# Performance work log

Measured on AMD Instinct MI355X. Metric: run time of the kernel, lower is better.

Reference implementation:

```python
import jax, jax.numpy as jnp
import numpy as np

# Dims: CrossMambaBlock(dim=256, H=32, W=32); inner Mamba(d_model=512, expand=1,
# d_state=16, bimamba_type='v2', if_devide_out=True, use_norm=True)
B, N, C = 4, 1024, 256
D_MODEL = 2 * C          # 512 (mamba d_model)
D_INNER = D_MODEL        # expand=1
D_STATE = 16
DT_RANK = 32             # ceil(512/16)
D_CONV = 4


def _ln(x, g, b, eps=1e-5):
    m = jnp.mean(x, axis=-1, keepdims=True)
    v = jnp.var(x, axis=-1, keepdims=True)
    return (x - m) * jax.lax.rsqrt(v + eps) * g + b


def _depthwise_causal_conv(x, w, b):
    # x: (B, d, L), w: (d, 1, k) -> causal conv (pad k-1 left), matches Conv1d(padding=k-1)[..., :L]
    y = jax.lax.conv_general_dilated(
        x, w, window_strides=(1,), padding=[(D_CONV - 1, 0)],
        feature_group_count=D_INNER, dimension_numbers=('NCH', 'OIH', 'NCH'))
    return y + b[None, :, None]


def _selective_scan(u, delta, A, Bm, Cm, Dv):
    # u, delta: (B, d, L); A: (d, n); Bm, Cm: (B, n, L); Dv: (d,)
    dA = jnp.exp(jnp.einsum('bdl,dn->lbdn', delta, A))
    dBu = jnp.einsum('bdl,bnl->lbdn', delta * u, Bm)
    Ct = jnp.transpose(Cm, (2, 0, 1))  # (L, B, n)

    def step(h, inp):
        dA_t, dBu_t, c_t = inp
        h = dA_t * h + dBu_t                          # (B, d, n)
        y = jnp.einsum('bdn,bn->bd', h, c_t)
        return h, y

    h0 = jnp.zeros((u.shape[0], u.shape[1], A.shape[1]), u.dtype)
    _, ys = jax.lax.scan(step, h0, (dA, dBu, Ct))
    y = jnp.transpose(ys, (1, 2, 0))                  # (B, d, L)
    return y + Dv[:, None] * u


def _mamba_dir(xz, conv_w, conv_b, xproj_w, dt_w, dt_b, A_log, Dv):
    x, z = jnp.split(xz, 2, axis=1)                   # each (B, d_inner, L)
    x = jax.nn.silu(_depthwise_causal_conv(x, conv_w, conv_b))
    x_dbl = jnp.einsum('bdl,ed->bel', x, xproj_w)     # (B, dt_rank+2n, L)
    dt = x_dbl[:, :DT_RANK]
    Bm = x_dbl[:, DT_RANK:DT_RANK + D_STATE]
    Cm = x_dbl[:, DT_RANK + D_STATE:]
    delta = jax.nn.softplus(jnp.einsum('brl,dr->bdl', dt, dt_w) + dt_b[None, :, None])
    A = -jnp.exp(A_log)
    y = _selective_scan(x, delta, A, Bm, Cm, Dv)
    return y * jax.nn.silu(z)                         # (B, d_inner, L)


def _forward(input0, input1, norm0_g, norm0_b, norm1_g, norm1_b, in_proj_w,
             convf_w, convf_b, convb_w, convb_b, xprojf_w, xprojb_w,
             dtf_w, dtf_b, dtb_w, dtb_b, A_log_f, A_log_b, D_f, D_b,
             mnorm_g, mnorm_b, outproj_w, pnorm_g, pnorm_b,
             projback_w, projback_b, cw_w, cw_b, cwln_g, cwln_b):
    i0 = jnp.nan_to_num(input0, nan=0.0, posinf=1.0, neginf=-1.0)
    i1 = jnp.nan_to_num(input1, nan=0.0, posinf=1.0, neginf=-1.0)
    skip = i0
    x0n = _ln(i0, norm0_g, norm0_b)
    x1n = _ln(i1, norm1_g, norm1_b)
    combined = jnp.concatenate([x0n, x1n], axis=-1)   # (B, N, 2C)
    weight = jax.nn.sigmoid(_ln(combined @ cw_w.T + cw_b, cwln_g, cwln_b))
    weight = jnp.clip(weight, 0.01, 0.99)
    # Mamba (bimamba v2): shared in_proj, two directional scans
    xz = jnp.einsum('bld,ed->bel', combined, in_proj_w)  # (B, 2*d_inner, L)
    out_f = _mamba_dir(xz, convf_w, convf_b, xprojf_w, dtf_w, dtf_b, A_log_f, D_f)
    out_b = _mamba_dir(jnp.flip(xz, -1), convb_w, convb_b, xprojb_w, dtb_w, dtb_b, A_log_b, D_b)
    y = (out_f + jnp.flip(out_b, -1)) * 0.5           # if_devide_out
    y = _ln(jnp.transpose(y, (0, 2, 1)), mnorm_g, mnorm_b)  # use_norm
    out = y @ outproj_w.T                              # (B, N, 2C)
    out = _ln(out, pnorm_g, pnorm_b)
    out = out @ projback_w.T + projback_b              # (B, N, C)
    out = jnp.nan_to_num(out, nan=0.0, posinf=1.0, neginf=-1.0)
    out = out * weight + x0n * (1.0 - weight)
    return out + skip


def setup_inputs() -> dict:
    key = jax.random.key(0)
    ks = iter(jax.random.split(key, 40))
    def rn(shape, s=0.02):
        return jax.random.normal(next(ks), shape, jnp.float32) * s
    inp = {}
    inp['input0'] = jax.random.normal(next(ks), (B, N, C), jnp.float32)
    inp['input1'] = jax.random.normal(next(ks), (B, N, C), jnp.float32)
    for nm in ['norm0', 'norm1']:
        inp[nm + '_g'] = jnp.ones((C,), jnp.float32)
        inp[nm + '_b'] = jnp.zeros((C,), jnp.float32)
    inp['in_proj_w'] = rn((2 * D_INNER, D_MODEL))
    for t in ['f', 'b']:
        inp['conv%s_w' % t] = rn((D_INNER, 1, D_CONV), 0.1)
        inp['conv%s_b' % t] = jnp.zeros((D_INNER,), jnp.float32)
        inp['xproj%s_w' % t] = rn((DT_RANK + 2 * D_STATE, D_INNER))
        inp['dt%s_w' % t] = rn((D_INNER, DT_RANK), 0.05)
        inp['dt%s_b' % t] = rn((D_INNER,), 0.05)
        inp['A_log_%s' % t] = jnp.log(jnp.broadcast_to(
            jnp.arange(1, D_STATE + 1, dtype=jnp.float32), (D_INNER, D_STATE)))
        inp['D_%s' % t] = jnp.ones((D_INNER,), jnp.float32)
    inp['mnorm_g'] = jnp.ones((D_INNER,), jnp.float32)
    inp['mnorm_b'] = jnp.zeros((D_INNER,), jnp.float32)
    inp['outproj_w'] = rn((D_MODEL, D_INNER))
    inp['pnorm_g'] = jnp.ones((D_MODEL,), jnp.float32)
    inp['pnorm_b'] = jnp.zeros((D_MODEL,), jnp.float32)
    inp['projback_w'] = rn((C, D_MODEL))
    inp['projback_b'] = jnp.zeros((C,), jnp.float32)
    inp['cw_w'] = rn((C, D_MODEL))
    inp['cw_b'] = jnp.zeros((C,), jnp.float32)
    inp['cwln_g'] = jnp.ones((C,), jnp.float32)
    inp['cwln_b'] = jnp.zeros((C,), jnp.float32)
    return inp


def reference(input0, input1, norm0_g, norm0_b, norm1_g, norm1_b, in_proj_w,
              convf_w, convf_b, convb_w, convb_b, xprojf_w, xprojb_w,
              dtf_w, dtf_b, dtb_w, dtb_b, A_log_f, A_log_b, D_f, D_b,
              mnorm_g, mnorm_b, outproj_w, pnorm_g, pnorm_b,
              projback_w, projback_b, cw_w, cw_b, cwln_g, cwln_b):
    return _forward(input0, input1, norm0_g, norm0_b, norm1_g, norm1_b, in_proj_w,
                    convf_w, convf_b, convb_w, convb_b, xprojf_w, xprojb_w,
                    dtf_w, dtf_b, dtb_w, dtb_b, A_log_f, A_log_b, D_f, D_b,
                    mnorm_g, mnorm_b, outproj_w, pnorm_g, pnorm_b,
                    projback_w, projback_b, cw_w, cw_b, cwln_g, cwln_b)
```

## Files before the change

kernel.cpp:

```cpp
#include <hip/hip_runtime.h>

#define BDIM 4
#define SEQ 1024
#define CH 256
#define DMODEL 512
#define DINNER 512
#define DSTATE 16
#define DTRANK 32
#define NROWS (BDIM * SEQ)
#define NCHUNK 32
#define CHUNK (SEQ / NCHUNK)

typedef unsigned short ushort_t;

__device__ __forceinline__ float nan2num(float x) {
    if (isnan(x)) return 0.f;
    if (isinf(x)) return x > 0.f ? 1.f : -1.f;
    return x;
}

__device__ __forceinline__ float silu_f(float x) { return x / (1.f + __expf(-x)); }
__device__ __forceinline__ float sigmoid_f(float x) { return 1.f / (1.f + __expf(-x)); }
__device__ __forceinline__ float softplus_f(float x) {
    return x > 20.f ? x : log1pf(__expf(x));
}

__device__ __forceinline__ ushort_t f2bf(float x) {
    union { float f; unsigned u; } v; v.f = x;
    unsigned r = v.u + 0x7fff + ((v.u >> 16) & 1);
    return (ushort_t)(r >> 16);
}
__device__ __forceinline__ float bf2f(ushort_t x) {
    union { unsigned u; float f; } v; v.u = ((unsigned)x) << 16;
    return v.f;
}

using bf16x8 = __attribute__((ext_vector_type(8))) __bf16;
using f32x4  = __attribute__((ext_vector_type(4))) float;

__device__ __forceinline__ void wave_reduce2(float& s, float& q) {
#pragma unroll
    for (int m = 32; m > 0; m >>= 1) {
        s += __shfl_xor(s, m);
        q += __shfl_xor(q, m);
    }
}

#define SZ_INPROJ (1024 * 512)
#define SZ_CW     (256 * 512)
#define SZ_XP     (64 * 512)
#define SZ_DT     (512 * 32)
#define SZ_OUTP   (512 * 512)
#define SZ_PROJB  (256 * 512)
#define SZ_WTOT   (SZ_INPROJ + SZ_CW + 2 * SZ_XP + 2 * SZ_DT + SZ_OUTP + SZ_PROJB)

__global__ __launch_bounds__(256) void convert_weights_kernel(
        const float* __restrict__ w0, const float* __restrict__ w1,
        const float* __restrict__ w2, const float* __restrict__ w3,
        const float* __restrict__ w4, const float* __restrict__ w5,
        const float* __restrict__ w6, const float* __restrict__ w7,
        ushort_t* __restrict__ out) {
    int i = blockIdx.x * 256 + threadIdx.x;
    if (i >= SZ_WTOT) return;
    int j = i;
    const float* src;
    if (j < SZ_INPROJ) { src = w0; }
    else { j -= SZ_INPROJ;
        if (j < SZ_CW) { src = w1; }
        else { j -= SZ_CW;
            if (j < SZ_XP) { src = w2; }
            else { j -= SZ_XP;
                if (j < SZ_XP) { src = w3; }
                else { j -= SZ_XP;
                    if (j < SZ_DT) { src = w4; }
                    else { j -= SZ_DT;
                        if (j < SZ_DT) { src = w5; }
                        else { j -= SZ_DT;
                            if (j < SZ_OUTP) { src = w6; }
                            else { j -= SZ_OUTP; src = w7; }
                        }
                    }
                }
            }
        }
    }
    out[i] = f2bf(src[j]);
}

__global__ __launch_bounds__(256) void ln01_kernel(
        const float* __restrict__ i0, const float* __restrict__ i1,
        const float* __restrict__ g0, const float* __restrict__ b0,
        const float* __restrict__ g1, const float* __restrict__ b1,
        float* __restrict__ x0n, ushort_t* __restrict__ combined) {
    int w = threadIdx.x >> 6, lane = threadIdx.x & 63;
    int row = blockIdx.x * 4 + w;

    float4 v = ((const float4*)(i0 + row * CH))[lane];
    v.x = nan2num(v.x); v.y = nan2num(v.y); v.z = nan2num(v.z); v.w = nan2num(v.w);
    float s = v.x + v.y + v.z + v.w;
    float q = v.x * v.x + v.y * v.y + v.z * v.z + v.w * v.w;
    wave_reduce2(s, q);
    float m = s / (float)CH;
    float r = rsqrtf(q / (float)CH - m * m + 1e-5f);
    float4 g = ((const float4*)g0)[lane];
    float4 bb = ((const float4*)b0)[lane];
    float4 o;
    o.x = (v.x - m) * r * g.x + bb.x;
    o.y = (v.y - m) * r * g.y + bb.y;
    o.z = (v.z - m) * r * g.z + bb.z;
    o.w = (v.w - m) * r * g.w + bb.w;
    ((float4*)(x0n + row * CH))[lane] = o;
    *(ushort4*)(combined + row * DMODEL + lane * 4) =
        make_ushort4(f2bf(o.x), f2bf(o.y), f2bf(o.z), f2bf(o.w));

    v = ((const float4*)(i1 + row * CH))[lane];
    v.x = nan2num(v.x); v.y = nan2num(v.y); v.z = nan2num(v.z); v.w = nan2num(v.w);
    s = v.x + v.y + v.z + v.w;
    q = v.x * v.x + v.y * v.y + v.z * v.z + v.w * v.w;
    wave_reduce2(s, q);
    m = s / (float)CH;
    r = rsqrtf(q / (float)CH - m * m + 1e-5f);
    g = ((const float4*)g1)[lane];
    bb = ((const float4*)b1)[lane];
    o.x = (v.x - m) * r * g.x + bb.x;
    o.y = (v.y - m) * r * g.y + bb.y;
    o.z = (v.z - m) * r * g.z + bb.z;
    o.w = (v.w - m) * r * g.w + bb.w;
    *(ushort4*)(combined + row * DMODEL + CH + lane * 4) =
        make_ushort4(f2bf(o.x), f2bf(o.y), f2bf(o.z), f2bf(o.w));
}

template<int ACT>
__global__ __launch_bounds__(256) void gemm64_kernel(
        const ushort_t* __restrict__ A0, const ushort_t* __restrict__ A1, int lda,
        const ushort_t* __restrict__ W0, const ushort_t* __restrict__ W1, int ldw,
        ushort_t* __restrict__ C0, ushort_t* __restrict__ C1, int ldc,
        int K, const float* __restrict__ bias0, const float* __restrict__ bias1) {
    const ushort_t* A = blockIdx.z ? A1 : A0;
    const ushort_t* W = blockIdx.z ? W1 : W0;
    ushort_t* C = blockIdx.z ? C1 : C0;
    const float* bias = blockIdx.z ? bias1 : bias0;

    __shared__ __align__(16) ushort_t As[64][40];
    __shared__ __align__(16) ushort_t Ws[64][40];
    const int t = threadIdx.x;
    const int m0 = blockIdx.y * 64;
    const int n0 = blockIdx.x * 64;
    const int w = t >> 6;
    const int lane = t & 63;
    const int lane16 = lane & 15;
    const int quad = lane >> 4;
    const int wr = (w >> 1) * 32;
    const int wc = (w & 1) * 32;
    const int srow = t >> 2;
    const int sc8 = (t & 3) * 8;

    f32x4 acc[2][2] = {};

    for (int k0 = 0; k0 < K; k0 += 32) {
        float4 av = *(const float4*)(A + (m0 + srow) * lda + k0 + sc8);
        float4 wv = *(const float4*)(W + (n0 + srow) * ldw + k0 + sc8);
        *(float4*)&As[srow][sc8] = av;
        *(float4*)&Ws[srow][sc8] = wv;
        __syncthreads();

        bf16x8 af[2], bfr[2];
#pragma unroll
        for (int i = 0; i < 2; ++i) {
            af[i]  = *(bf16x8*)&As[wr + i * 16 + lane16][quad * 8];
            bfr[i] = *(bf16x8*)&Ws[wc + i * 16 + lane16][quad * 8];
        }
#pragma unroll
        for (int i = 0; i < 2; ++i)
#pragma unroll
            for (int j = 0; j < 2; ++j)
                acc[i][j] = __builtin_amdgcn_mfma_f32_16x16x32_bf16(af[i], bfr[j], acc[i][j], 0, 0, 0);
        __syncthreads();
    }

#pragma unroll
    for (int j = 0; j < 2; ++j) {
        int col = n0 + wc + j * 16 + lane16;
        float bv = bias ? bias[col] : 0.f;
#pragma unroll
        for (int i = 0; i < 2; ++i) {
#pragma unroll
            for (int r = 0; r < 4; ++r) {
                int row = m0 + wr + i * 16 + quad * 4 + r;
                float c = acc[i][j][r] + bv;
                if (ACT == 1) c = softplus_f(c);
                C[row * ldc + col] = f2bf(c);
            }
        }
    }
}

template<int ACT>
__global__ __launch_bounds__(256) void gemm128_kernel(
        const ushort_t* __restrict__ A0, const ushort_t* __restrict__ A1, int lda,
        const ushort_t* __restrict__ W0, const ushort_t* __restrict__ W1, int ldw,
        ushort_t* __restrict__ C0, ushort_t* __restrict__ C1, int ldc,
        int K, const float* __restrict__ bias0, const float* __restrict__ bias1) {
    const ushort_t* A = blockIdx.z ? A1 : A0;
    const ushort_t* W = blockIdx.z ? W1 : W0;
    ushort_t* C = blockIdx.z ? C1 : C0;
    const float* bias = blockIdx.z ? bias1 : bias0;

    __shared__ __align__(16) ushort_t As[128][40];
    __shared__ __align__(16) ushort_t Ws[64][40];
    const int t = threadIdx.x;
    const int m0 = blockIdx.y * 128;
    const int n0 = blockIdx.x * 64;
    const int w = t >> 6;
    const int lane = t & 63;
    const int lane16 = lane & 15;
    const int quad = lane >> 4;
    const int wr = (w >> 1) * 64;
    const int wc = (w & 1) * 32;
    const int arow = t >> 1;
    const int ac = (t & 1) * 16;
    const int srow = t >> 2;
    const int sc8 = (t & 3) * 8;

    f32x4 acc[4][2] = {};

    for (int k0 = 0; k0 < K; k0 += 32) {
        float4 a0 = *(const float4*)(A + (m0 + arow) * lda + k0 + ac);
        float4 a1 = *(const float4*)(A + (m0 + arow) * lda + k0 + ac + 8);
        float4 wv = *(const float4*)(W + (n0 + srow) * ldw + k0 + sc8);
        *(float4*)&As[arow][ac] = a0;
        *(float4*)&As[arow][ac + 8] = a1;
        *(float4*)&Ws[srow][sc8] = wv;
        __syncthreads();

        bf16x8 af[4], bfr[2];
#pragma unroll
        for (int i = 0; i < 4; ++i)
            af[i] = *(bf16x8*)&As[wr + i * 16 + lane16][quad * 8];
#pragma unroll
        for (int j = 0; j < 2; ++j)
            bfr[j] = *(bf16x8*)&Ws[wc + j * 16 + lane16][quad * 8];
#pragma unroll
        for (int i = 0; i < 4; ++i)
#pragma unroll
            for (int j = 0; j < 2; ++j)
                acc[i][j] = __builtin_amdgcn_mfma_f32_16x16x32_bf16(af[i], bfr[j], acc[i][j], 0, 0, 0);
        __syncthreads();
    }

#pragma unroll
    for (int j = 0; j < 2; ++j) {
        int col = n0 + wc + j * 16 + lane16;
        float bv = bias ? bias[col] : 0.f;
#pragma unroll
        for (int i = 0; i < 4; ++i) {
#pragma unroll
            for (int r = 0; r < 4; ++r) {
                int row = m0 + wr + i * 16 + quad * 4 + r;
                float c = acc[i][j][r] + bv;
                if (ACT == 1) c = softplus_f(c);
                C[row * ldc + col] = f2bf(c);
            }
        }
    }
}

__global__ __launch_bounds__(256) void gemm_projback_final_kernel(
        const ushort_t* __restrict__ A, int lda,
        const ushort_t* __restrict__ W, int ldw,
        int K, const float* __restrict__ bias,
        const ushort_t* __restrict__ wgt, const float* __restrict__ x0n,
        const float* __restrict__ i0, float* __restrict__ out) {
    __shared__ __align__(16) ushort_t As[64][40];
    __shared__ __align__(16) ushort_t Ws[64][40];
    const int t = threadIdx.x;
    const int m0 = blockIdx.y * 64;
    const int n0 = blockIdx.x * 64;
    const int w = t >> 6;
    const int lane = t & 63;
    const int lane16 = lane & 15;
    const int quad = lane >> 4;
    const int wr = (w >> 1) * 32;
    const int wc = (w & 1) * 32;
    const int srow = t >> 2;
    const int sc8 = (t & 3) * 8;

    f32x4 acc[2][2] = {};

    for (int k0 = 0; k0 < K; k0 += 32) {
        float4 av = *(const float4*)(A + (m0 + srow) * lda + k0 + sc8);
        float4 wv = *(const float4*)(W + (n0 + srow) * ldw + k0 + sc8);
        *(float4*)&As[srow][sc8] = av;
        *(float4*)&Ws[srow][sc8] = wv;
        __syncthreads();

        bf16x8 af[2], bfr[2];
#pragma unroll
        for (int i = 0; i < 2; ++i) {
            af[i]  = *(bf16x8*)&As[wr + i * 16 + lane16][quad * 8];
            bfr[i] = *(bf16x8*)&Ws[wc + i * 16 + lane16][quad * 8];
        }
#pragma unroll
        for (int i = 0; i < 2; ++i)
#pragma unroll
            for (int j = 0; j < 2; ++j)
                acc[i][j] = __builtin_amdgcn_mfma_f32_16x16x32_bf16(af[i], bfr[j], acc[i][j], 0, 0, 0);
        __syncthreads();
    }

#pragma unroll
    for (int j = 0; j < 2; ++j) {
        int col = n0 + wc + j * 16 + lane16;
        float bv = bias[col];
#pragma unroll
        for (int i = 0; i < 2; ++i) {
#pragma unroll
            for (int r = 0; r < 4; ++r) {
                int row = m0 + wr + i * 16 + quad * 4 + r;
                float o = nan2num(acc[i][j][r] + bv);
                float wv = bf2f(wgt[row * CH + col]);
                float xv = x0n[row * CH + col];
                float sk = nan2num(i0[row * CH + col]);
                out[row * CH + col] = o * wv + xv * (1.f - wv) + sk;
            }
        }
    }
}

__global__ __launch_bounds__(256) void weight_ln_kernel(
        ushort_t* __restrict__ wbuf, const float* __restrict__ g, const float* __restrict__ b) {
    int w = threadIdx.x >> 6, lane = threadIdx.x & 63;
    int row = blockIdx.x * 4 + w;
    ushort4 raw = *(const ushort4*)(wbuf + row * CH + lane * 4);
    float4 v = make_float4(bf2f(raw.x), bf2f(raw.y), bf2f(raw.z), bf2f(raw.w));
    float s = v.x + v.y + v.z + v.w;
    float q = v.x * v.x + v.y * v.y + v.z * v.z + v.w * v.w;
    wave_reduce2(s, q);
    float m = s / (float)CH;
    float r = rsqrtf(q / (float)CH - m * m + 1e-5f);
    float4 g4 = ((const float4*)g)[lane];
    float4 b4 = ((const float4*)b)[lane];
    float ox = fminf(fmaxf(sigmoid_f((v.x - m) * r * g4.x + b4.x), 0.01f), 0.99f);
    float oy = fminf(fmaxf(sigmoid_f((v.y - m) * r * g4.y + b4.y), 0.01f), 0.99f);
    float oz = fminf(fmaxf(sigmoid_f((v.z - m) * r * g4.z + b4.z), 0.01f), 0.99f);
    float ow = fminf(fmaxf(sigmoid_f((v.w - m) * r * g4.w + b4.w), 0.01f), 0.99f);
    *(ushort4*)(wbuf + row * CH + lane * 4) = make_ushort4(f2bf(ox), f2bf(oy), f2bf(oz), f2bf(ow));
}

__global__ __launch_bounds__(256) void conv_both_kernel(
        const ushort_t* __restrict__ xz,
        const float* __restrict__ wf, const float* __restrict__ wbf,
        const float* __restrict__ wb, const float* __restrict__ wbb,
        ushort_t* __restrict__ outf, ushort_t* __restrict__ outb) {
    const int t = threadIdx.x;
    const int lane = t & 127;
    const int row = blockIdx.x * 2 + (t >> 7);
    const int l = row & (SEQ - 1);
    const int b = row >> 10;
    const int d0 = lane * 4;

    float x[7][4];
#pragma unroll
    for (int j = 0; j < 7; ++j) {
        int ll = l - 3 + j;
        if (ll >= 0 && ll < SEQ) {
            ushort4 raw = *(const ushort4*)(xz + (b * SEQ + ll) * (2 * DINNER) + d0);
            x[j][0] = bf2f(raw.x); x[j][1] = bf2f(raw.y);
            x[j][2] = bf2f(raw.z); x[j][3] = bf2f(raw.w);
        } else {
#pragma unroll
            for (int k = 0; k < 4; ++k) x[j][k] = 0.f;
        }
    }

    float wfv[16], wbv[16];
#pragma unroll
    for (int qq = 0; qq < 4; ++qq) {
        float4 a = *(const float4*)(wf + d0 * 4 + qq * 4);
        wfv[qq * 4] = a.x; wfv[qq * 4 + 1] = a.y; wfv[qq * 4 + 2] = a.z; wfv[qq * 4 + 3] = a.w;
        float4 c = *(const float4*)(wb + d0 * 4 + qq * 4);
        wbv[qq * 4] = c.x; wbv[qq * 4 + 1] = c.y; wbv[qq * 4 + 2] = c.z; wbv[qq * 4 + 3] = c.w;
    }
    float4 bfv = *(const float4*)(wbf + d0);
    float4 bbv = *(const float4*)(wbb + d0);
    float biasf[4] = {bfv.x, bfv.y, bfv.z, bfv.w};
    float biasb[4] = {bbv.x, bbv.y, bbv.z, bbv.w};

    ushort_t of[4], ob[4];
#pragma unroll
    for (int qq = 0; qq < 4; ++qq) {
        float accf = biasf[qq], accb = biasb[qq];
#pragma unroll
        for (int k = 0; k < 4; ++k) {
            accf += x[k][qq] * wfv[qq * 4 + k];
            accb += x[6 - k][qq] * wbv[qq * 4 + k];
        }
        of[qq] = f2bf(silu_f(accf));
        ob[qq] = f2bf(silu_f(accb));
    }
    *(ushort4*)(outf + row * DINNER + d0) = make_ushort4(of[0], of[1], of[2], of[3]);
    *(ushort4*)(outb + (b * SEQ + (SEQ - 1 - l)) * DINNER + d0) =
        make_ushort4(ob[0], ob[1], ob[2], ob[3]);
}

__global__ __launch_bounds__(256) void scan_pass1_kernel(
        const ushort_t* __restrict__ df, const ushort_t* __restrict__ db,
        const ushort_t* __restrict__ uf, const ushort_t* __restrict__ ub,
        const ushort_t* __restrict__ xf, const ushort_t* __restrict__ xb,
        const float* __restrict__ Alf, const float* __restrict__ Alb,
        float* __restrict__ cAf, float* __restrict__ cAb,
        float* __restrict__ cHf, float* __restrict__ cHb) {
    const int dir = blockIdx.z >> 2;
    const int b = blockIdx.z & 3;
    const ushort_t* delta = dir ? db : df;
    const ushort_t* u     = dir ? ub : uf;
    const ushort_t* xdbl  = dir ? xb : xf;
    const float* A_log    = dir ? Alb : Alf;
    float* chunkA = dir ? cAb : cAf;
    float* chunkH = dir ? cHb : cHf;

    const int c = blockIdx.y;
    const int d = blockIdx.x * 256 + threadIdx.x;
    const int base = b * SEQ + c * CHUNK;

    __shared__ float sB[CHUNK][16];
    {
        int t = threadIdx.x;
        if (t < CHUNK * 2) {
            int row = t >> 1, f8 = (t & 1) * 8;
            float4 raw = *(const float4*)(xdbl + (base + row) * 64 + DTRANK + f8);
            const ushort_t* us = (const ushort_t*)&raw;
#pragma unroll
            for (int k = 0; k < 8; ++k) sB[row][f8 + k] = bf2f(us[k]);
        }
    }
    __syncthreads();

    float a[DSTATE];
#pragma unroll
    for (int n = 0; n < DSTATE; n += 4) {
        float4 al = *(const float4*)(A_log + d * DSTATE + n);
        a[n] = -__expf(al.x); a[n + 1] = -__expf(al.y);
        a[n + 2] = -__expf(al.z); a[n + 3] = -__expf(al.w);
    }
    float h[DSTATE];
#pragma unroll
    for (int n = 0; n < DSTATE; ++n) h[n] = 0.f;

    float sumdl = 0.f;
    for (int s = 0; s < CHUNK; ++s) {
        int row = base + s;
        float dl = bf2f(delta[row * DINNER + d]);
        float ul = bf2f(u[row * DINNER + d]);
        float dlul = dl * ul;
        sumdl += dl;
#pragma unroll
        for (int g = 0; g < 4; ++g) {
            float4 B4 = *(const float4*)&sB[s][g * 4];
            float dA0 = __expf(dl * a[g * 4 + 0]);
            float dA1 = __expf(dl * a[g * 4 + 1]);
            float dA2 = __expf(dl * a[g * 4 + 2]);
            float dA3 = __expf(dl * a[g * 4 + 3]);
            h[g * 4 + 0] = dA0 * h[g * 4 + 0] + dlul * B4.x;
            h[g * 4 + 1] = dA1 * h[g * 4 + 1] + dlul * B4.y;
            h[g * 4 + 2] = dA2 * h[g * 4 + 2] + dlul * B4.z;
            h[g * 4 + 3] = dA3 * h[g * 4 + 3] + dlul * B4.w;
        }
    }

    int idx = ((b * NCHUNK + c) * DINNER + d) * DSTATE;
#pragma unroll
    for (int n = 0; n < DSTATE; n += 4) {
        float4 P4 = make_float4(__expf(a[n] * sumdl), __expf(a[n + 1] * sumdl),
                                __expf(a[n + 2] * sumdl), __expf(a[n + 3] * sumdl));
        *(float4*)(chunkA + idx + n) = P4;
        *(float4*)(chunkH + idx + n) = make_float4(h[n], h[n + 1], h[n + 2], h[n + 3]);
    }
}

__global__ __launch_bounds__(256) void scan_pass2_kernel(
        const float* __restrict__ cAf, const float* __restrict__ cAb,
        float* __restrict__ cHf, float* __restrict__ cHb) {
    int tid = blockIdx.x * 256 + threadIdx.x;
    int dir = tid >> 15;
    int rr = tid & 32767;
    int b = rr >> 13;
    int rem = rr & 8191;
    const float* chunkA = dir ? cAb : cAf;
    float* chunkH = dir ? cHb : cHf;
    float h = 0.f;
    for (int c = 0; c < NCHUNK; ++c) {
        int idx = (b * NCHUNK + c) * (DINNER * DSTATE) + rem;
        float Ac = chunkA[idx];
        float Hc = chunkH[idx];
        chunkH[idx] = h;
        h = Ac * h + Hc;
    }
}

__global__ __launch_bounds__(256) void scan_pass3_kernel(
        const ushort_t* __restrict__ df, const ushort_t* __restrict__ db,
        const ushort_t* __restrict__ uf, const ushort_t* __restrict__ ub,
        const ushort_t* __restrict__ xf, const ushort_t* __restrict__ xb,
        const float* __restrict__ Alf, const float* __restrict__ Alb,
        const float* __restrict__ Dvf, const float* __restrict__ Dvb,
        const float* __restrict__ hfb, const float* __restrict__ hbb,
        ushort_t* __restrict__ yfo, ushort_t* __restrict__ ybo) {
    const int dir = blockIdx.z >> 2;
    const int b = blockIdx.z & 3;
    const ushort_t* delta = dir ? db : df;
    const ushort_t* u     = dir ? ub : uf;
    const ushort_t* xdbl  = dir ? xb : xf;
    const float* A_log    = dir ? Alb : Alf;
    const float* Dv       = dir ? Dvb : Dvf;
    const float* hin      = dir ? hbb : hfb;
    ushort_t* yout        = dir ? ybo : yfo;

    const int c = blockIdx.y;
    const int d = blockIdx.x * 256 + threadIdx.x;
    const int base = b * SEQ + c * CHUNK;

    __shared__ float sBC[CHUNK][32];
    {
        int t = threadIdx.x;
        if (t < CHUNK * 4) {
            int row = t >> 2, f8 = (t & 3) * 8;
            float4 raw = *(const float4*)(xdbl + (base + row) * 64 + DTRANK + f8);
            const ushort_t* us = (const ushort_t*)&raw;
#pragma unroll
            for (int k = 0; k < 8; ++k) sBC[row][f8 + k] = bf2f(us[k]);
        }
    }
    __syncthreads();

    float a[DSTATE];
#pragma unroll
    for (int n = 0; n < DSTATE; n += 4) {
        float4 al = *(const float4*)(A_log + d * DSTATE + n);
        a[n] = -__expf(al.x); a[n + 1] = -__expf(al.y);
        a[n + 2] = -__expf(al.z); a[n + 3] = -__expf(al.w);
    }
    float h[DSTATE];
    {
        int idx = ((b * NCHUNK + c) * DINNER + d) * DSTATE;
#pragma unroll
        for (int n = 0; n < DSTATE; n += 4) {
            float4 h4 = *(const float4*)(hin + idx + n);
            h[n] = h4.x; h[n + 1] = h4.y; h[n + 2] = h4.z; h[n + 3] = h4.w;
        }
    }
    const float Dd = Dv[d];

    for (int s = 0; s < CHUNK; ++s) {
        int row = base + s;
        float dl = bf2f(delta[row * DINNER + d]);
        float ul = bf2f(u[row * DINNER + d]);
        float dlul = dl * ul;
        float y = 0.f;
#pragma unroll
        for (int g = 0; g < 4; ++g) {
            float4 B4 = *(const float4*)&sBC[s][g * 4];
            float4 C4 = *(const float4*)&sBC[s][16 + g * 4];
            float dA0 = __expf(dl * a[g * 4 + 0]);
            float dA1 = __expf(dl * a[g * 4 + 1]);
            float dA2 = __expf(dl * a[g * 4 + 2]);
            float dA3 = __expf(dl * a[g * 4 + 3]);
            h[g * 4 + 0] = dA0 * h[g * 4 + 0] + dlul * B4.x;
            h[g * 4 + 1] = dA1 * h[g * 4 + 1] + dlul * B4.y;
            h[g * 4 + 2] = dA2 * h[g * 4 + 2] + dlul * B4.z;
            h[g * 4 + 3] = dA3 * h[g * 4 + 3] + dlul * B4.w;
            y += h[g * 4 + 0] * C4.x + h[g * 4 + 1] * C4.y
               + h[g * 4 + 2] * C4.z + h[g * 4 + 3] * C4.w;
        }
        int lpos = c * CHUNK + s;
        int orow = b * SEQ + (dir ? (SEQ - 1 - lpos) : lpos);
        yout[orow * DINNER + d] = f2bf(y + Dd * ul);
    }
}

__global__ __launch_bounds__(256) void combine_mnorm_kernel(
        const ushort_t* __restrict__ yf, const ushort_t* __restrict__ yb,
        const ushort_t* __restrict__ xz,
        const float* __restrict__ g, const float* __restrict__ b,
        ushort_t* __restrict__ yn) {
    int w = threadIdx.x >> 6, lane = threadIdx.x & 63;
    int row = blockIdx.x * 4 + w;
    float4 rf = *(const float4*)(yf + row * DINNER + lane * 8);
    float4 rb = *(const float4*)(yb + row * DINNER + lane * 8);
    float4 rz = *(const float4*)(xz + row * (2 * DINNER) + DINNER + lane * 8);
    const ushort_t* uf = (const ushort_t*)&rf;
    const ushort_t* ub = (const ushort_t*)&rb;
    const ushort_t* uz = (const ushort_t*)&rz;
    float v[8];
    float s = 0.f, q = 0.f;
#pragma unroll
    for (int k = 0; k < 8; ++k) {
        float val = 0.5f * (bf2f(uf[k]) + bf2f(ub[k])) * silu_f(bf2f(uz[k]));
        v[k] = val; s += val; q += val * val;
    }
    wave_reduce2(s, q);
    float m = s / (float)DINNER;
    float r = rsqrtf(q / (float)DINNER - m * m + 1e-5f);
    ushort_t o[8];
#pragma unroll
    for (int k = 0; k < 8; ++k)
        o[k] = f2bf((v[k] - m) * r * g[lane * 8 + k] + b[lane * 8 + k]);
    *(ushort4*)(yn + row * DINNER + lane * 8) = make_ushort4(o[0], o[1], o[2], o[3]);
    *(ushort4*)(yn + row * DINNER + lane * 8 + 4) = make_ushort4(o[4], o[5], o[6], o[7]);
}

__global__ __launch_bounds__(256) void ln512_kernel(
        const ushort_t* __restrict__ in,
        const float* __restrict__ g, const float* __restrict__ b,
        ushort_t* __restrict__ out) {
    int w = threadIdx.x >> 6, lane = threadIdx.x & 63;
    int row = blockIdx.x * 4 + w;
    float4 raw = *(const float4*)(in + row * DMODEL + lane * 8);
    const ushort_t* us = (const ushort_t*)&raw;
    float v[8];
    float s = 0.f, q = 0.f;
#pragma unroll
    for (int k = 0; k < 8; ++k) {
        v[k] = bf2f(us[k]); s += v[k]; q += v[k] * v[k];
    }
    wave_reduce2(s, q);
    float m = s / (float)DMODEL;
    float r = rsqrtf(q / (float)DMODEL - m * m + 1e-5f);
    ushort_t o[8];
#pragma unroll
    for (int k = 0; k < 8; ++k)
        o[k] = f2bf((v[k] - m) * r * g[lane * 8 + k] + b[lane * 8 + k]);
    *(ushort4*)(out + row * DMODEL + lane * 8) = make_ushort4(o[0], o[1], o[2], o[3]);
    *(ushort4*)(out + row * DMODEL + lane * 8 + 4) = make_ushort4(o[4], o[5], o[6], o[7]);
}

extern "C" void kernel_launch(void* const* d_in, const int* in_sizes, int n_in,
                              void* d_out, int out_size, void* d_ws, size_t ws_size,
                              hipStream_t stream) {
    (void)in_sizes; (void)n_in; (void)out_size; (void)ws_size;
    const float* input0    = (const float*)d_in[0];
    const float* input1    = (const float*)d_in[1];
    const float* norm0_g   = (const float*)d_in[2];
    const float* norm0_b   = (const float*)d_in[3];
    const float* norm1_g   = (const float*)d_in[4];
    const float* norm1_b   = (const float*)d_in[5];
    const float* in_proj_w = (const float*)d_in[6];
    const float* convf_w   = (const float*)d_in[7];
    const float* convf_b   = (const float*)d_in[8];
    const float* xprojf_w  = (const float*)d_in[9];
    const float* dtf_w     = (const float*)d_in[10];
    const float* dtf_b     = (const float*)d_in[11];
    const float* A_log_f   = (const float*)d_in[12];
    const float* D_f       = (const float*)d_in[13];
    const float* convb_w   = (const float*)d_in[14];
    const float* convb_b   = (const float*)d_in[15];
    const float* xprojb_w  = (const float*)d_in[16];
    const float* dtb_w     = (const float*)d_in[17];
    const float* dtb_b     = (const float*)d_in[18];
    const float* A_log_b   = (const float*)d_in[19];
    const float* D_b       = (const float*)d_in[20];
    const float* mnorm_g   = (const float*)d_in[21];
    const float* mnorm_b   = (const float*)d_in[22];
    const float* outproj_w = (const float*)d_in[23];
    const float* pnorm_g   = (const float*)d_in[24];
    const float* pnorm_b   = (const float*)d_in[25];
    const float* projback_w= (const float*)d_in[26];
    const float* projback_b= (const float*)d_in[27];
    const float* cw_w      = (const float*)d_in[28];
    const float* cw_b      = (const float*)d_in[29];
    const float* cwln_g    = (const float*)d_in[30];
    const float* cwln_b    = (const float*)d_in[31];

    float* wsf = (float*)d_ws;
    float* x0n      = wsf;
    float* chunkA_f = x0n + 1048576;
    float* chunkA_b = chunkA_f + 1048576;
    float* chunkH_f = chunkA_b + 1048576;
    float* chunkH_b = chunkH_f + 1048576;
    ushort_t* wsu = (ushort_t*)(chunkH_b + 1048576);
    ushort_t* combined = wsu;
    ushort_t* xz       = combined + 2097152;
    ushort_t* weight   = xz + 4194304;
    ushort_t* xdbl_f   = weight + 1048576;
    ushort_t* xdbl_b   = xdbl_f + 262144;
    ushort_t* xconv_f  = xdbl_b + 262144;
    ushort_t* xconv_b  = xconv_f + 2097152;
    ushort_t* delta_f  = xconv_b + 2097152;
    ushort_t* delta_b  = delta_f + 2097152;
    ushort_t* y_f      = delta_b + 2097152;
    ushort_t* y_b      = y_f + 2097152;
    ushort_t* yn       = y_b + 2097152;
    ushort_t* o1       = yn + 2097152;
    ushort_t* on1      = o1 + 2097152;
    ushort_t* wb       = on1 + 2097152;
    ushort_t* w_inproj = wb;
    ushort_t* w_cw     = w_inproj + SZ_INPROJ;
    ushort_t* w_xpf    = w_cw + SZ_CW;
    ushort_t* w_xpb    = w_xpf + SZ_XP;
    ushort_t* w_dtf    = w_xpb + SZ_XP;
    ushort_t* w_dtb    = w_dtf + SZ_DT;
    ushort_t* w_outp   = w_dtb + SZ_DT;
    ushort_t* w_projb  = w_outp + SZ_OUTP;

    convert_weights_kernel<<<(SZ_WTOT + 255) / 256, 256, 0, stream>>>(
        in_proj_w, cw_w, xprojf_w, xprojb_w, dtf_w, dtb_w, outproj_w, projback_w, wb);

    ln01_kernel<<<NROWS / 4, 256, 0, stream>>>(input0, input1, norm0_g, norm0_b,
                                               norm1_g, norm1_b, x0n, combined);

    gemm128_kernel<0><<<dim3(16, 32, 1), 256, 0, stream>>>(
        combined, combined, DMODEL, w_inproj, w_inproj, DMODEL,
        xz, xz, 2 * DINNER, DMODEL, nullptr, nullptr);

    gemm64_kernel<0><<<dim3(4, 64, 1), 256, 0, stream>>>(
        combined, combined, DMODEL, w_cw, w_cw, DMODEL,
        weight, weight, CH, DMODEL, cw_b, cw_b);

    weight_ln_kernel<<<NROWS / 4, 256, 0, stream>>>(weight, cwln_g, cwln_b);

    conv_both_kernel<<<NROWS / 2, 256, 0, stream>>>(
        xz, convf_w, convf_b, convb_w, convb_b, xconv_f, xconv_b);

    gemm64_kernel<0><<<dim3(1, 64, 2), 256, 0, stream>>>(
        xconv_f, xconv_b, DINNER, w_xpf, w_xpb, DINNER,
        xdbl_f, xdbl_b, 64, DINNER, nullptr, nullptr);

    gemm128_kernel<1><<<dim3(8, 32, 2), 256, 0, stream>>>(
        xdbl_f, xdbl_b, 64, w_dtf, w_dtb, DTRANK,
        delta_f, delta_b, DINNER, DTRANK, dtf_b, dtb_b);

    dim3 sgrid(DINNER / 256, NCHUNK, 2 * BDIM);
    scan_pass1_kernel<<<sgrid, 256, 0, stream>>>(
        delta_f, delta_b, xconv_f, xconv_b, xdbl_f, xdbl_b, A_log_f, A_log_b,
        chunkA_f, chunkA_b, chunkH_f, chunkH_b);
    scan_pass2_kernel<<<256, 256, 0, stream>>>(chunkA_f, chunkA_b, chunkH_f, chunkH_b);
    scan_pass3_kernel<<<sgrid, 256, 0, stream>>>(
        delta_f, delta_b, xconv_f, xconv_b, xdbl_f, xdbl_b, A_log_f, A_log_b,
        D_f, D_b, chunkH_f, chunkH_b, y_f, y_b);

    combine_mnorm_kernel<<<NROWS / 4, 256, 0, stream>>>(y_f, y_b, xz, mnorm_g, mnorm_b, yn);

    gemm128_kernel<0><<<dim3(8, 32, 1), 256, 0, stream>>>(
        yn, yn, DINNER, w_outp, w_outp, DINNER,
        o1, o1, DMODEL, DINNER, nullptr, nullptr);

    ln512_kernel<<<NROWS / 4, 256, 0, stream>>>(o1, pnorm_g, pnorm_b, on1);

    gemm_projback_final_kernel<<<dim3(4, 64, 1), 256, 0, stream>>>(
        on1, DMODEL, w_projb, DMODEL, DMODEL, projback_b,
        weight, x0n, input0, (float*)d_out);
}
```

Baseline: 270.6 us.

## Fuse delta projection into scan passes and merge small pre-processing launches

The dt-projection GEMM and softplus are now computed inside both scan passes from the xdbl rows staged in shared memory, so the bf16 delta buffers are never written or read. The weight conversion and input LayerNorm share one launch, the in_proj and cw GEMMs share one launch through the z dimension with an early exit for the narrower one, and the weight LayerNorm is folded into the conv launch. This removes several launches and a large intermediate round trip, at the cost of recomputing the 32-wide dot product in both pass1 and pass3 and holding 32 extra registers per thread.

```diff
diff --git a/kernel.cpp b/kernel.cpp
--- a/kernel.cpp
+++ b/kernel.cpp
@@ -53,45 +53,48 @@
 #define SZ_OUTP   (512 * 512)
 #define SZ_PROJB  (256 * 512)
 #define SZ_WTOT   (SZ_INPROJ + SZ_CW + 2 * SZ_XP + 2 * SZ_DT + SZ_OUTP + SZ_PROJB)
-
-__global__ __launch_bounds__(256) void convert_weights_kernel(
+#define LN01_BLOCKS (NROWS / 4)
+#define CVT_BLOCKS  ((SZ_WTOT + 255) / 256)
+
+__global__ __launch_bounds__(256) void fused_pre_kernel(
+        const float* __restrict__ i0, const float* __restrict__ i1,
+        const float* __restrict__ g0, const float* __restrict__ b0,
+        const float* __restrict__ g1, const float* __restrict__ b1,
+        float* __restrict__ x0n, ushort_t* __restrict__ combined,
         const float* __restrict__ w0, const float* __restrict__ w1,
         const float* __restrict__ w2, const float* __restrict__ w3,
         const float* __restrict__ w4, const float* __restrict__ w5,
         const float* __restrict__ w6, const float* __restrict__ w7,
-        ushort_t* __restrict__ out) {
-    int i = blockIdx.x * 256 + threadIdx.x;
-    if (i >= SZ_WTOT) return;
-    int j = i;
-    const float* src;
-    if (j < SZ_INPROJ) { src = w0; }
-    else { j -= SZ_INPROJ;
-        if (j < SZ_CW) { src = w1; }
-        else { j -= SZ_CW;
-            if (j < SZ_XP) { src = w2; }
-            else { j -= SZ_XP;
-                if (j < SZ_XP) { src = w3; }
+        ushort_t* __restrict__ wout) {
+    if (blockIdx.x >= LN01_BLOCKS) {
+        int i = (blockIdx.x - LN01_BLOCKS) * 256 + threadIdx.x;
+        if (i >= SZ_WTOT) return;
+        int j = i;
+        const float* src;
+        if (j < SZ_INPROJ) { src = w0; }
+        else { j -= SZ_INPROJ;
+            if (j < SZ_CW) { src = w1; }
+            else { j -= SZ_CW;
+                if (j < SZ_XP) { src = w2; }
                 else { j -= SZ_XP;
-                    if (j < SZ_DT) { src = w4; }
-                    else { j -= SZ_DT;
-                        if (j < SZ_DT) { src = w5; }
+                    if (j < SZ_XP) { src = w3; }
+                    else { j -= SZ_XP;
+                        if (j < SZ_DT) { src = w4; }
                         else { j -= SZ_DT;
-                            if (j < SZ_OUTP) { src = w6; }
-                            else { j -= SZ_OUTP; src = w7; }
+                            if (j < SZ_DT) { src = w5; }
+                            else { j -= SZ_DT;
+                                if (j < SZ_OUTP) { src = w6; }
+                                else { j -= SZ_OUTP; src = w7; }
+                            }
                         }
                     }
                 }
             }
         }
-    }
-    out[i] = f2bf(src[j]);
-}
-
-__global__ __launch_bounds__(256) void ln01_kernel(
-        const float* __restrict__ i0, const float* __restrict__ i1,
-        const float* __restrict__ g0, const float* __restrict__ b0,
-        const float* __restrict__ g1, const float* __restrict__ b1,
-        float* __restrict__ x0n, ushort_t* __restrict__ combined) {
+        wout[i] = f2bf(src[j]);
+        return;
+    }
+
     int w = threadIdx.x >> 6, lane = threadIdx.x & 63;
     int row = blockIdx.x * 4 + w;
 
@@ -131,79 +134,17 @@
 }
 
 template<int ACT>
-__global__ __launch_bounds__(256) void gemm64_kernel(
+__global__ __launch_bounds__(256) void gemm128_kernel(
         const ushort_t* __restrict__ A0, const ushort_t* __restrict__ A1, int lda,
         const ushort_t* __restrict__ W0, const ushort_t* __restrict__ W1, int ldw,
-        ushort_t* __restrict__ C0, ushort_t* __restrict__ C1, int ldc,
-        int K, const float* __restrict__ bias0, const float* __restrict__ bias1) {
+        ushort_t* __restrict__ C0, ushort_t* __restrict__ C1, int ldc0, int ldc1,
+        int K, const float* __restrict__ bias0, const float* __restrict__ bias1,
+        int nx1) {
+    if (blockIdx.z && (int)blockIdx.x >= nx1) return;
     const ushort_t* A = blockIdx.z ? A1 : A0;
     const ushort_t* W = blockIdx.z ? W1 : W0;
     ushort_t* C = blockIdx.z ? C1 : C0;
-    const float* bias = blockIdx.z ? bias1 : bias0;
-
-    __shared__ __align__(16) ushort_t As[64][40];
-    __shared__ __align__(16) ushort_t Ws[64][40];
-    const int t = threadIdx.x;
-    const int m0 = blockIdx.y * 64;
-    const int n0 = blockIdx.x * 64;
-    const int w = t >> 6;
-    const int lane = t & 63;
-    const int lane16 = lane & 15;
-    const int quad = lane >> 4;
-    const int wr = (w >> 1) * 32;
-    const int wc = (w & 1) * 32;
-    const int srow = t >> 2;
-    const int sc8 = (t & 3) * 8;
-
-    f32x4 acc[2][2] = {};
-
-    for (int k0 = 0; k0 < K; k0 += 32) {
-        float4 av = *(const float4*)(A + (m0 + srow) * lda + k0 + sc8);
-        float4 wv = *(const float4*)(W + (n0 + srow) * ldw + k0 + sc8);
-        *(float4*)&As[srow][sc8] = av;
-        *(float4*)&Ws[srow][sc8] = wv;
-        __syncthreads();
-
-        bf16x8 af[2], bfr[2];
-#pragma unroll
-        for (int i = 0; i < 2; ++i) {
-            af[i]  = *(bf16x8*)&As[wr + i * 16 + lane16][quad * 8];
-            bfr[i] = *(bf16x8*)&Ws[wc + i * 16 + lane16][quad * 8];
-        }
-#pragma unroll
-        for (int i = 0; i < 2; ++i)
-#pragma unroll
-            for (int j = 0; j < 2; ++j)
-                acc[i][j] = __builtin_amdgcn_mfma_f32_16x16x32_bf16(af[i], bfr[j], acc[i][j], 0, 0, 0);
-        __syncthreads();
-    }
-
-#pragma unroll
-    for (int j = 0; j < 2; ++j) {
-        int col = n0 + wc + j * 16 + lane16;
-        float bv = bias ? bias[col] : 0.f;
-#pragma unroll
-        for (int i = 0; i < 2; ++i) {
-#pragma unroll
-            for (int r = 0; r < 4; ++r) {
-                int row = m0 + wr + i * 16 + quad * 4 + r;
-                float c = acc[i][j][r] + bv;
-                if (ACT == 1) c = softplus_f(c);
-                C[row * ldc + col] = f2bf(c);
-            }
-        }
-    }
-}
-
-template<int ACT>
-__global__ __launch_bounds__(256) void gemm128_kernel(
-        const ushort_t* __restrict__ A0, const ushort_t* __restrict__ A1, int lda,
-        const ushort_t* __restrict__ W0, const ushort_t* __restrict__ W1, int ldw,
-        ushort_t* __restrict__ C0, ushort_t* __restrict__ C1, int ldc,
-        int K, const float* __restrict__ bias0, const float* __restrict__ bias1) {
-    const ushort_t* A = blockIdx.z ? A1 : A0;
-    const ushort_t* W = blockIdx.z ? W1 : W0;
-    ushort_t* C = blockIdx.z ? C1 : C0;
+    const int ldc = blockIdx.z ? ldc1 : ldc0;
     const float* bias = blockIdx.z ? bias1 : bias0;
 
     __shared__ __align__(16) ushort_t As[128][40];
@@ -254,6 +195,71 @@
         float bv = bias ? bias[col] : 0.f;
 #pragma unroll
         for (int i = 0; i < 4; ++i) {
+#pragma unroll
+            for (int r = 0; r < 4; ++r) {
+                int row = m0 + wr + i * 16 + quad * 4 + r;
+                float c = acc[i][j][r] + bv;
+                if (ACT == 1) c = softplus_f(c);
+                C[row * ldc + col] = f2bf(c);
+            }
+        }
+    }
+}
+
+template<int ACT>
+__global__ __launch_bounds__(256) void gemm64_kernel(
+        const ushort_t* __restrict__ A0, const ushort_t* __restrict__ A1, int lda,
+        const ushort_t* __restrict__ W0, const ushort_t* __restrict__ W1, int ldw,
+        ushort_t* __restrict__ C0, ushort_t* __restrict__ C1, int ldc,
+        int K, const float* __restrict__ bias0, const float* __restrict__ bias1) {
+    const ushort_t* A = blockIdx.z ? A1 : A0;
+    const ushort_t* W = blockIdx.z ? W1 : W0;
+    ushort_t* C = blockIdx.z ? C1 : C0;
+    const float* bias = blockIdx.z ? bias1 : bias0;
+
+    __shared__ __align__(16) ushort_t As[64][40];
+    __shared__ __align__(16) ushort_t Ws[64][40];
+    const int t = threadIdx.x;
+    const int m0 = blockIdx.y * 64;
+    const int n0 = blockIdx.x * 64;
+    const int w = t >> 6;
+    const int lane = t & 63;
+    const int lane16 = lane & 15;
+    const int quad = lane >> 4;
+    const int wr = (w >> 1) * 32;
+    const int wc = (w & 1) * 32;
+    const int srow = t >> 2;
+    const int sc8 = (t & 3) * 8;
+
+    f32x4 acc[2][2] = {};
+
+    for (int k0 = 0; k0 < K; k0 += 32) {
+        float4 av = *(const float4*)(A + (m0 + srow) * lda + k0 + sc8);
+        float4 wv = *(const float4*)(W + (n0 + srow) * ldw + k0 + sc8);
+        *(float4*)&As[srow][sc8] = av;
+        *(float4*)&Ws[srow][sc8] = wv;
+        __syncthreads();
+
+        bf16x8 af[2], bfr[2];
+#pragma unroll
+        for (int i = 0; i < 2; ++i) {
+            af[i]  = *(bf16x8*)&As[wr + i * 16 + lane16][quad * 8];
+            bfr[i] = *(bf16x8*)&Ws[wc + i * 16 + lane16][quad * 8];
+        }
+#pragma unroll
+        for (int i = 0; i < 2; ++i)
+#pragma unroll
+            for (int j = 0; j < 2; ++j)
+                acc[i][j] = __builtin_amdgcn_mfma_f32_16x16x32_bf16(af[i], bfr[j], acc[i][j], 0, 0, 0);
+        __syncthreads();
+    }
+
+#pragma unroll
+    for (int j = 0; j < 2; ++j) {
+        int col = n0 + wc + j * 16 + lane16;
+        float bv = bias ? bias[col] : 0.f;
+#pragma unroll
+        for (int i = 0; i < 2; ++i) {
 #pragma unroll
             for (int r = 0; r < 4; ++r) {
                 int row = m0 + wr + i * 16 + quad * 4 + r;
@@ -327,32 +333,33 @@
     }
 }
 
-__global__ __launch_bounds__(256) void weight_ln_kernel(
-        ushort_t* __restrict__ wbuf, const float* __restrict__ g, const float* __restrict__ b) {
-    int w = threadIdx.x >> 6, lane = threadIdx.x & 63;
-    int row = blockIdx.x * 4 + w;
-    ushort4 raw = *(const ushort4*)(wbuf + row * CH + lane * 4);
-    float4 v = make_float4(bf2f(raw.x), bf2f(raw.y), bf2f(raw.z), bf2f(raw.w));
-    float s = v.x + v.y + v.z + v.w;
-    float q = v.x * v.x + v.y * v.y + v.z * v.z + v.w * v.w;
-    wave_reduce2(s, q);
-    float m = s / (float)CH;
-    float r = rsqrtf(q / (float)CH - m * m + 1e-5f);
-    float4 g4 = ((const float4*)g)[lane];
-    float4 b4 = ((const float4*)b)[lane];
-    float ox = fminf(fmaxf(sigmoid_f((v.x - m) * r * g4.x + b4.x), 0.01f), 0.99f);
-    float oy = fminf(fmaxf(sigmoid_f((v.y - m) * r * g4.y + b4.y), 0.01f), 0.99f);
-    float oz = fminf(fmaxf(sigmoid_f((v.z - m) * r * g4.z + b4.z), 0.01f), 0.99f);
-    float ow = fminf(fmaxf(sigmoid_f((v.w - m) * r * g4.w + b4.w), 0.01f), 0.99f);
-    *(ushort4*)(wbuf + row * CH + lane * 4) = make_ushort4(f2bf(ox), f2bf(oy), f2bf(oz), f2bf(ow));
-}
-
-__global__ __launch_bounds__(256) void conv_both_kernel(
+__global__ __launch_bounds__(256) void conv_wln_kernel(
         const ushort_t* __restrict__ xz,
         const float* __restrict__ wf, const float* __restrict__ wbf,
         const float* __restrict__ wb, const float* __restrict__ wbb,
-        ushort_t* __restrict__ outf, ushort_t* __restrict__ outb) {
+        ushort_t* __restrict__ outf, ushort_t* __restrict__ outb,
+        ushort_t* __restrict__ wbuf, const float* __restrict__ cg,
+        const float* __restrict__ cb) {
     const int t = threadIdx.x;
+    if (blockIdx.x >= NROWS / 2) {
+        int w = t >> 6, lane = t & 63;
+        int row = (blockIdx.x - NROWS / 2) * 4 + w;
+        ushort4 raw = *(const ushort4*)(wbuf + row * CH + lane * 4);
+        float4 v = make_float4(bf2f(raw.x), bf2f(raw.y), bf2f(raw.z), bf2f(raw.w));
+        float s = v.x + v.y + v.z + v.w;
+        float q = v.x * v.x + v.y * v.y + v.z * v.z + v.w * v.w;
+        wave_reduce2(s, q);
+        float m = s / (float)CH;
+        float r = rsqrtf(q / (float)CH - m * m + 1e-5f);
+        float4 g4 = ((const float4*)cg)[lane];
+        float4 b4 = ((const float4*)cb)[lane];
+        float ox = fminf(fmaxf(sigmoid_f((v.x - m) * r * g4.x + b4.x), 0.01f), 0.99f);
+        float oy = fminf(fmaxf(sigmoid_f((v.y - m) * r * g4.y + b4.y), 0.01f), 0.99f);
+        float oz = fminf(fmaxf(sigmoid_f((v.z - m) * r * g4.z + b4.z), 0.01f), 0.99f);
+        float ow = fminf(fmaxf(sigmoid_f((v.w - m) * r * g4.w + b4.w), 0.01f), 0.99f);
+        *(ushort4*)(wbuf + row * CH + lane * 4) = make_ushort4(f2bf(ox), f2bf(oy), f2bf(oz), f2bf(ow));
+        return;
+    }
     const int lane = t & 127;
     const int row = blockIdx.x * 2 + (t >> 7);
     const int l = row & (SEQ - 1);
@@ -404,18 +411,20 @@
 }
 
 __global__ __launch_bounds__(256) void scan_pass1_kernel(
-        const ushort_t* __restrict__ df, const ushort_t* __restrict__ db,
         const ushort_t* __restrict__ uf, const ushort_t* __restrict__ ub,
         const ushort_t* __restrict__ xf, const ushort_t* __restrict__ xb,
+        const ushort_t* __restrict__ dtwf, const ushort_t* __restrict__ dtwb,
+        const float* __restrict__ dtbf, const float* __restrict__ dtbb,
         const float* __restrict__ Alf, const float* __restrict__ Alb,
         float* __restrict__ cAf, float* __restrict__ cAb,
         float* __restrict__ cHf, float* __restrict__ cHb) {
     const int dir = blockIdx.z >> 2;
     const int b = blockIdx.z & 3;
-    const ushort_t* delta = dir ? db : df;
-    const ushort_t* u     = dir ? ub : uf;
-    const ushort_t* xdbl  = dir ? xb : xf;
-    const float* A_log    = dir ? Alb : Alf;
+    const ushort_t* u    = dir ? ub : uf;
+    const ushort_t* xdbl = dir ? xb : xf;
+    const ushort_t* dtw  = dir ? dtwb : dtwf;
+    const float* dtbias  = dir ? dtbb : dtbf;
+    const float* A_log   = dir ? Alb : Alf;
     float* chunkA = dir ? cAb : cAf;
     float* chunkH = dir ? cHb : cHf;
 
@@ -423,18 +432,26 @@
     const int d = blockIdx.x * 256 + threadIdx.x;
     const int base = b * SEQ + c * CHUNK;
 
-    __shared__ float sB[CHUNK][16];
+    __shared__ float sX[CHUNK][64];
     {
         int t = threadIdx.x;
-        if (t < CHUNK * 2) {
-            int row = t >> 1, f8 = (t & 1) * 8;
-            float4 raw = *(const float4*)(xdbl + (base + row) * 64 + DTRANK + f8);
-            const ushort_t* us = (const ushort_t*)&raw;
-#pragma unroll
-            for (int k = 0; k < 8; ++k) sB[row][f8 + k] = bf2f(us[k]);
-        }
+        int row = t >> 3, oct = (t & 7) * 8;
+        float4 raw = *(const float4*)(xdbl + (base + row) * 64 + oct);
+        const ushort_t* us = (const ushort_t*)&raw;
+#pragma unroll
+        for (int k = 0; k < 8; ++k) sX[row][oct + k] = bf2f(us[k]);
     }
     __syncthreads();
+
+    float dtv[32];
+#pragma unroll
+    for (int r8 = 0; r8 < 4; ++r8) {
+        float4 raw = *(const float4*)(dtw + d * DTRANK + r8 * 8);
+        const ushort_t* us = (const ushort_t*)&raw;
+#pragma unroll
+        for (int k = 0; k < 8; ++k) dtv[r8 * 8 + k] = bf2f(us[k]);
+    }
+    const float dtb0 = dtbias[d];
 
     float a[DSTATE];
 #pragma unroll
@@ -449,14 +466,20 @@
 
     float sumdl = 0.f;
     for (int s = 0; s < CHUNK; ++s) {
-        int row = base + s;
-        float dl = bf2f(delta[row * DINNER + d]);
-        float ul = bf2f(u[row * DINNER + d]);
+        float acc = dtb0;
+#pragma unroll
+        for (int g = 0; g < 8; ++g) {
+            float4 xr = *(const float4*)&sX[s][g * 4];
+            acc += xr.x * dtv[g * 4] + xr.y * dtv[g * 4 + 1]
+                 + xr.z * dtv[g * 4 + 2] + xr.w * dtv[g * 4 + 3];
+        }
+        float dl = softplus_f(acc);
+        float ul = bf2f(u[(base + s) * DINNER + d]);
         float dlul = dl * ul;
         sumdl += dl;
 #pragma unroll
         for (int g = 0; g < 4; ++g) {
-            float4 B4 = *(const float4*)&sB[s][g * 4];
+            float4 B4 = *(const float4*)&sX[s][32 + g * 4];
             float dA0 = __expf(dl * a[g * 4 + 0]);
             float dA1 = __expf(dl * a[g * 4 + 1]);
             float dA2 = __expf(dl * a[g * 4 + 2]);
@@ -499,39 +522,49 @@
 }
 
 __global__ __launch_bounds__(256) void scan_pass3_kernel(
-        const ushort_t* __restrict__ df, const ushort_t* __restrict__ db,
         const ushort_t* __restrict__ uf, const ushort_t* __restrict__ ub,
         const ushort_t* __restrict__ xf, const ushort_t* __restrict__ xb,
+        const ushort_t* __restrict__ dtwf, const ushort_t* __restrict__ dtwb,
+        const float* __restrict__ dtbf, const float* __restrict__ dtbb,
         const float* __restrict__ Alf, const float* __restrict__ Alb,
         const float* __restrict__ Dvf, const float* __restrict__ Dvb,
         const float* __restrict__ hfb, const float* __restrict__ hbb,
         ushort_t* __restrict__ yfo, ushort_t* __restrict__ ybo) {
     const int dir = blockIdx.z >> 2;
     const int b = blockIdx.z & 3;
-    const ushort_t* delta = dir ? db : df;
-    const ushort_t* u     = dir ? ub : uf;
-    const ushort_t* xdbl  = dir ? xb : xf;
-    const float* A_log    = dir ? Alb : Alf;
-    const float* Dv       = dir ? Dvb : Dvf;
-    const float* hin      = dir ? hbb : hfb;
-    ushort_t* yout        = dir ? ybo : yfo;
+    const ushort_t* u    = dir ? ub : uf;
+    const ushort_t* xdbl = dir ? xb : xf;
+    const ushort_t* dtw  = dir ? dtwb : dtwf;
+    const float* dtbias  = dir ? dtbb : dtbf;
+    const float* A_log   = dir ? Alb : Alf;
+    const float* Dv      = dir ? Dvb : Dvf;
+    const float* hin     = dir ? hbb : hfb;
+    ushort_t* yout       = dir ? ybo : yfo;
 
     const int c = blockIdx.y;
     const int d = blockIdx.x * 256 + threadIdx.x;
     const int base = b * SEQ + c * CHUNK;
 
-    __shared__ float sBC[CHUNK][32];
+    __shared__ float sX[CHUNK][64];
     {
         int t = threadIdx.x;
-        if (t < CHUNK * 4) {
-            int row = t >> 2, f8 = (t & 3) * 8;
-            float4 raw = *(const float4*)(xdbl + (base + row) * 64 + DTRANK + f8);
-            const ushort_t* us = (const ushort_t*)&raw;
-#pragma unroll
-            for (int k = 0; k < 8; ++k) sBC[row][f8 + k] = bf2f(us[k]);
-        }
+        int row = t >> 3, oct = (t & 7) * 8;
+        float4 raw = *(const float4*)(xdbl + (base + row) * 64 + oct);
+        const ushort_t* us = (const ushort_t*)&raw;
+#pragma unroll
+        for (int k = 0; k < 8; ++k) sX[row][oct + k] = bf2f(us[k]);
     }
     __syncthreads();
+
+    float dtv[32];
+#pragma unroll
+    for (int r8 = 0; r8 < 4; ++r8) {
+        float4 raw = *(const float4*)(dtw + d * DTRANK + r8 * 8);
+        const ushort_t* us = (const ushort_t*)&raw;
+#pragma unroll
+        for (int k = 0; k < 8; ++k) dtv[r8 * 8 + k] = bf2f(us[k]);
+    }
+    const float dtb0 = dtbias[d];
 
     float a[DSTATE];
 #pragma unroll
@@ -552,15 +585,21 @@
     const float Dd = Dv[d];
 
     for (int s = 0; s < CHUNK; ++s) {
-        int row = base + s;
-        float dl = bf2f(delta[row * DINNER + d]);
-        float ul = bf2f(u[row * DINNER + d]);
+        float acc = dtb0;
+#pragma unroll
+        for (int g = 0; g < 8; ++g) {
+            float4 xr = *(const float4*)&sX[s][g * 4];
+            acc += xr.x * dtv[g * 4] + xr.y * dtv[g * 4 + 1]
+                 + xr.z * dtv[g * 4 + 2] + xr.w * dtv[g * 4 + 3];
+        }
+        float dl = softplus_f(acc);
+        float ul = bf2f(u[(base + s) * DINNER + d]);
         float dlul = dl * ul;
         float y = 0.f;
 #pragma unroll
         for (int g = 0; g < 4; ++g) {
-            float4 B4 = *(const float4*)&sBC[s][g * 4];
-            float4 C4 = *(const float4*)&sBC[s][16 + g * 4];
+            float4 B4 = *(const float4*)&sX[s][32 + g * 4];
+            float4 C4 = *(const float4*)&sX[s][48 + g * 4];
             float dA0 = __expf(dl * a[g * 4 + 0]);
             float dA1 = __expf(dl * a[g * 4 + 1]);
             float dA2 = __expf(dl * a[g * 4 + 2]);
@@ -685,9 +724,7 @@
     ushort_t* xdbl_b   = xdbl_f + 262144;
     ushort_t* xconv_f  = xdbl_b + 262144;
     ushort_t* xconv_b  = xconv_f + 2097152;
-    ushort_t* delta_f  = xconv_b + 2097152;
-    ushort_t* delta_b  = delta_f + 2097152;
-    ushort_t* y_f      = delta_b + 2097152;
+    ushort_t* y_f      = xconv_b + 2097152;
     ushort_t* y_b      = y_f + 2097152;
     ushort_t* yn       = y_b + 2097152;
     ushort_t* o1       = yn + 2097152;
@@ -702,47 +739,36 @@
     ushort_t* w_outp   = w_dtb + SZ_DT;
     ushort_t* w_projb  = w_outp + SZ_OUTP;
 
-    convert_weights_kernel<<<(SZ_WTOT + 255) / 256, 256, 0, stream>>>(
+    fused_pre_kernel<<<LN01_BLOCKS + CVT_BLOCKS, 256, 0, stream>>>(
+        input0, input1, norm0_g, norm0_b, norm1_g, norm1_b, x0n, combined,
         in_proj_w, cw_w, xprojf_w, xprojb_w, dtf_w, dtb_w, outproj_w, projback_w, wb);
 
-    ln01_kernel<<<NROWS / 4, 256, 0, stream>>>(input0, input1, norm0_g, norm0_b,
-                                               norm1_g, norm1_b, x0n, combined);
-
-    gemm128_kernel<0><<<dim3(16, 32, 1), 256, 0, stream>>>(
-        combined, combined, DMODEL, w_inproj, w_inproj, DMODEL,
-        xz, xz, 2 * DINNER, DMODEL, nullptr, nullptr);
-
-    gemm64_kernel<0><<<dim3(4, 64, 1), 256, 0, stream>>>(
-        combined, combined, DMODEL, w_cw, w_cw, DMODEL,
-        weight, weight, CH, DMODEL, cw_b, cw_b);
-
-    weight_ln_kernel<<<NROWS / 4, 256, 0, stream>>>(weight, cwln_g, cwln_b);
-
-    conv_both_kernel<<<NROWS / 2, 256, 0, stream>>>(
-        xz, convf_w, convf_b, convb_w, convb_b, xconv_f, xconv_b);
+    gemm128_kernel<0><<<dim3(16, 32, 2), 256, 0, stream>>>(
+        combined, combined, DMODEL, w_inproj, w_cw, DMODEL,
+        xz, weight, 2 * DINNER, CH, DMODEL, nullptr, cw_b, 4);
+
+    conv_wln_kernel<<<NROWS / 2 + NROWS / 4, 256, 0, stream>>>(
+        xz, convf_w, convf_b, convb_w, convb_b, xconv_f, xconv_b,
+        weight, cwln_g, cwln_b);
 
     gemm64_kernel<0><<<dim3(1, 64, 2), 256, 0, stream>>>(
         xconv_f, xconv_b, DINNER, w_xpf, w_xpb, DINNER,
         xdbl_f, xdbl_b, 64, DINNER, nullptr, nullptr);
 
-    gemm128_kernel<1><<<dim3(8, 32, 2), 256, 0, stream>>>(
-        xdbl_f, xdbl_b, 64, w_dtf, w_dtb, DTRANK,
-        delta_f, delta_b, DINNER, DTRANK, dtf_b, dtb_b);
-
     dim3 sgrid(DINNER / 256, NCHUNK, 2 * BDIM);
     scan_pass1_kernel<<<sgrid, 256, 0, stream>>>(
-        delta_f, delta_b, xconv_f, xconv_b, xdbl_f, xdbl_b, A_log_f, A_log_b,
-        chunkA_f, chunkA_b, chunkH_f, chunkH_b);
+        xconv_f, xconv_b, xdbl_f, xdbl_b, w_dtf, w_dtb, dtf_b, dtb_b,
+        A_log_f, A_log_b, chunkA_f, chunkA_b, chunkH_f, chunkH_b);
     scan_pass2_kernel<<<256, 256, 0, stream>>>(chunkA_f, chunkA_b, chunkH_f, chunkH_b);
     scan_pass3_kernel<<<sgrid, 256, 0, stream>>>(
-        delta_f, delta_b, xconv_f, xconv_b, xdbl_f, xdbl_b, A_log_f, A_log_b,
-        D_f, D_b, chunkH_f, chunkH_b, y_f, y_b);
+        xconv_f, xconv_b, xdbl_f, xdbl_b, w_dtf, w_dtb, dtf_b, dtb_b,
+        A_log_f, A_log_b, D_f, D_b, chunkH_f, chunkH_b, y_f, y_b);
 
     combine_mnorm_kernel<<<NROWS / 4, 256, 0, stream>>>(y_f, y_b, xz, mnorm_g, mnorm_b, yn);
 
     gemm128_kernel<0><<<dim3(8, 32, 1), 256, 0, stream>>>(
         yn, yn, DINNER, w_outp, w_outp, DINNER,
-        o1, o1, DMODEL, DINNER, nullptr, nullptr);
+        o1, o1, DMODEL, DMODEL, DINNER, nullptr, nullptr, 8);
 
     ln512_kernel<<<NROWS / 4, 256, 0, stream>>>(o1, pnorm_g, pnorm_b, on1);
 
```

After: 278.5 us. 1.03x slower.
